# Kernel optimization log

Measured on AMD Instinct MI355X. Metric: run time of the kernel, lower is better.

The kernel has to match this reference:

```python
import jax, jax.numpy as jnp
import numpy as np

B = 8            # graphs per batch
NUM_NODES = 12500  # nodes per graph
N = B * NUM_NODES  # 100000 total nodes
E = 1_600_000      # edges (avg degree 16)
F_IN = 128
HID = 128


def _glorot(key, shape):
    lim = np.sqrt(6.0 / (shape[0] + shape[1])).astype(np.float32)
    return jax.random.uniform(key, shape, jnp.float32, -lim, lim)


def setup_inputs() -> dict:
    key = jax.random.key(0)
    ks = jax.random.split(key, 8)
    x = jax.random.normal(ks[0], (N, F_IN), jnp.float32)
    edge_index = jax.random.randint(ks[1], (2, E), 0, N, jnp.int32)
    batch = jnp.repeat(jnp.arange(B, dtype=jnp.int32), NUM_NODES)
    W1 = _glorot(ks[2], (F_IN, HID)); b1 = jnp.zeros((HID,), jnp.float32)
    W2 = _glorot(ks[3], (HID, HID));  b2 = jnp.zeros((HID,), jnp.float32)
    W3 = _glorot(ks[4], (HID, 1));    b3 = jnp.zeros((1,), jnp.float32)
    return {"x": x, "edge_index": edge_index, "batch": batch,
            "W1": W1, "b1": b1, "W2": W2, "b2": b2, "W3": W3, "b3": b3}


def _gcn_norm(src, dst, n):
    """Add self-loops and compute symmetric D^-1/2 A D^-1/2 edge weights (PyG GCNConv default)."""
    loop = jnp.arange(n, dtype=src.dtype)
    s = jnp.concatenate([src, loop])
    d = jnp.concatenate([dst, loop])
    deg = jax.ops.segment_sum(jnp.ones(s.shape[0], jnp.float32), d, num_segments=n)
    dinv = jnp.where(deg > 0, jax.lax.rsqrt(deg), 0.0)
    return s, d, dinv[s] * dinv[d]


def _gcn_conv(h, W, b, s, d, norm, n):
    h = h @ W                                   # [n, out]
    msg = h[s] * norm[:, None]                  # gather + scale
    out = jax.ops.segment_sum(msg, d, num_segments=n)  # scatter-add
    return out + b


def reference(x, edge_index, batch, W1, b1, W2, b2, W3, b3):
    n = x.shape[0]
    x_last = x[:, -1]                           # == x.view(B,NUM_NODES,F)[:,:,-1] flattened
    s, d, norm = _gcn_norm(edge_index[0], edge_index[1], n)
    h = jax.nn.relu(_gcn_conv(x, W1, b1, s, d, norm, n))   # dropout is identity in eval mode
    h = jax.nn.relu(_gcn_conv(h, W2, b2, s, d, norm, n))
    h = jax.nn.relu(_gcn_conv(h, W3, b3, s, d, norm, n))   # [n, 1]
    x_res = h.reshape(B, NUM_NODES)
    return x_res + x_last.reshape(B, NUM_NODES)
```

## Files before the change

kernel.cpp:

```cpp
#include <hip/hip_runtime.h>
#include <hip/hip_bf16.h>

typedef __attribute__((ext_vector_type(8))) short short8;
typedef __attribute__((ext_vector_type(8))) __bf16 bf16x8;
typedef __attribute__((ext_vector_type(4))) float f32x4;

static __device__ __forceinline__ float bflo(unsigned u){ return __uint_as_float(u << 16); }
static __device__ __forceinline__ float bfhi(unsigned u){ return __uint_as_float(u & 0xffff0000u); }
static __device__ __forceinline__ unsigned short f2bf(float f){
  unsigned u = __float_as_uint(f);
  unsigned r = u + 0x7fffu + ((u >> 16) & 1u);
  return (unsigned short)(r >> 16);
}

#if __has_builtin(__builtin_amdgcn_cvt_pk_fp8_f32)
static __device__ __forceinline__ unsigned char f2e4m3(float f){
  return (unsigned char)(__builtin_amdgcn_cvt_pk_fp8_f32(f, 0.f, 0, false) & 0xff);
}
#else
static __device__ __forceinline__ unsigned char f2e4m3(float f){
  unsigned s = (__float_as_uint(f) >> 31) << 7;
  float a = fabsf(f);
  if (a >= 448.f) return (unsigned char)(s | 0x7e);
  if (a < 0.0009765625f) return (unsigned char)s;
  if (a >= 0.015625f){
    int e; float m = frexpf(a, &e);
    int q = (int)rintf(m * 16.f);
    int E = e - 1 + 7;
    if (q == 16){ q = 8; E++; }
    if (E >= 16) return (unsigned char)(s | 0x7e);
    return (unsigned char)(s | (E << 3) | (q - 8));
  } else {
    int q = (int)rintf(a * 512.f);
    if (q > 7) return (unsigned char)(s | 0x08);
    return (unsigned char)(s | q);
  }
}
#endif

#if __has_builtin(__builtin_amdgcn_cvt_pk_f32_fp8)
static __device__ __forceinline__ float4 e4m3x4_to_f32(unsigned u){
  auto lo = __builtin_amdgcn_cvt_pk_f32_fp8((int)u, false);
  auto hi = __builtin_amdgcn_cvt_pk_f32_fp8((int)u, true);
  return make_float4(lo[0], lo[1], hi[0], hi[1]);
}
#else
static __device__ __forceinline__ float e4m3_1(unsigned b){
  unsigned s = b >> 7, e = (b >> 3) & 15, m = b & 7;
  float v = e ? ldexpf((float)(8 + m) * 0.125f, (int)e - 7) : ldexpf((float)m * 0.125f, -6);
  return s ? -v : v;
}
static __device__ __forceinline__ float4 e4m3x4_to_f32(unsigned u){
  return make_float4(e4m3_1(u & 255), e4m3_1((u >> 8) & 255), e4m3_1((u >> 16) & 255), e4m3_1(u >> 24));
}
#endif

static __device__ __forceinline__ void add8(float* acc, uint2 u){
  float4 a = e4m3x4_to_f32(u.x), b = e4m3x4_to_f32(u.y);
  acc[0] += a.x; acc[1] += a.y; acc[2] += a.z; acc[3] += a.w;
  acc[4] += b.x; acc[5] += b.y; acc[6] += b.z; acc[7] += b.w;
}

#define NBMAX  1024
#define PART_C 4096
#define STCAP  4096
#define BCAP   6144


__global__ __launch_bounds__(1024) void k_part(const int* __restrict__ src, const int* __restrict__ dst,
    int* __restrict__ bpos, unsigned* __restrict__ ebuf, int E, int NB)
{
  __shared__ int hist[NBMAX + 1];
  __shared__ int hist2[NBMAX];
  __shared__ int gbase[NBMAX];
  __shared__ int sc[1024];
  __shared__ unsigned staged[PART_C];
  __shared__ unsigned short sbkt[PART_C];

  const int t = threadIdx.x;
  const int base = blockIdx.x * PART_C;

  for (int i = t; i < NBMAX; i += 1024){ hist[i] = 0; hist2[i] = 0; }
  __syncthreads();

  unsigned up[4];
  int bb[4];
  #pragma unroll
  for (int j = 0; j < 4; j++){
    int e = base + j * 1024 + t;
    if (e < E){
      int s = src[e], d = dst[e];
      bb[j] = d >> 7;
      up[j] = ((unsigned)s << 7) | (unsigned)(d & 127);
      atomicAdd(&hist[bb[j]], 1);
    } else bb[j] = -1;
  }
  __syncthreads();

  int v = (t < NB) ? hist[t] : 0;
  sc[t] = v; __syncthreads();
  for (int off = 1; off < 1024; off <<= 1){
    int u = (t >= off) ? sc[t - off] : 0;
    __syncthreads();
    sc[t] += u;
    __syncthreads();
  }
  int incl = sc[t];
  if (t < NB) hist[t] = incl - v;
  if (t == NB - 1) hist[NB] = incl;
  if (t < NB && v > 0) gbase[t] = t * BCAP + atomicAdd(&bpos[t], v);
  __syncthreads();

  #pragma unroll
  for (int j = 0; j < 4; j++){
    if (bb[j] >= 0){
      int r = atomicAdd(&hist2[bb[j]], 1);
      int p = hist[bb[j]] + r;
      staged[p] = up[j];
      sbkt[p] = (unsigned short)bb[j];
    }
  }
  __syncthreads();

  int total = hist[NB];
  for (int i = t; i < total; i += 1024){
    int b = sbkt[i];
    ebuf[gbase[b] + (i - hist[b])] = staged[i];
  }
}

__global__ __launch_bounds__(256) void k_bsort(const unsigned* __restrict__ ebuf, const int* __restrict__ cnts,
    int* __restrict__ rowptr, int* __restrict__ colv, float* __restrict__ dinv, int n, int E, int NB)
{
  __shared__ int cl[128];
  __shared__ int sc2[256];
  __shared__ unsigned stg[STCAP];

  const int t = threadIdx.x;
  const int b = blockIdx.x;
  const int r0 = b << 7;
  const int rbeg = b * BCAP;
  const int total = cnts[b];

  {
    int psum = 0;
    for (int i = t; i < b; i += 256) psum += cnts[i];
    sc2[t] = psum; __syncthreads();
    for (int off = 128; off; off >>= 1){
      if (t < off) sc2[t] += sc2[t + off];
      __syncthreads();
    }
  }
  const int wbeg = sc2[0];
  __syncthreads();

  if (b == NB - 1 && t == 0) rowptr[n] = E;

  if (t < 128) cl[t] = 0;
  __syncthreads();
  for (int i = t; i < total; i += 256) atomicAdd(&cl[ebuf[rbeg + i] & 127u], 1);
  __syncthreads();

  int v = (t < 128) ? cl[t] : 0;
  sc2[t] = v; __syncthreads();
  for (int off = 1; off < 256; off <<= 1){
    int u = (t >= off) ? sc2[t - off] : 0;
    __syncthreads();
    sc2[t] += u;
    __syncthreads();
  }
  int excl = sc2[t] - v;
  if (t < 128){
    int node = r0 + t;
    if (node < n){
      rowptr[node] = wbeg + excl;
      dinv[node]   = rsqrtf((float)(v + 1));
    }
    cl[t] = excl;
  }
  __syncthreads();

  if (total <= STCAP){
    for (int i = t; i < total; i += 256){
      unsigned u = ebuf[rbeg + i];
      int p = atomicAdd(&cl[u & 127u], 1);
      stg[p] = u >> 7;
    }
    __syncthreads();
    for (int i = t; i < total; i += 256) colv[wbeg + i] = (int)stg[i];
  } else {
    for (int i = t; i < total; i += 256){
      unsigned u = ebuf[rbeg + i];
      int p = atomicAdd(&cl[u & 127u], 1);
      colv[wbeg + p] = (int)(u >> 7);
    }
  }
}


template<bool AF32>
__global__ __launch_bounds__(512) void k_gemm_mfma(const void* __restrict__ Ain, const float* __restrict__ W,
    const float* __restrict__ dinv, unsigned char* __restrict__ G8, int n)
{
  __shared__ unsigned short At[128 * 136];
  __shared__ float dl[128];

  const int t = threadIdx.x;
  const int rowBase = blockIdx.x * 128;
  const int w  = t >> 6;
  const int l  = t & 63;
  const int ln = l & 15;
  const int lg = l >> 4;

  if (t < 128){
    int gr = rowBase + t;
    dl[t] = (gr < n) ? dinv[gr] : 0.f;
  }

  #pragma unroll
  for (int i = 0; i < 4; i++){
    int flat = i * 4096 + t * 8;
    int r = flat >> 7, c = flat & 127;
    int gr = rowBase + r;
    unsigned short tmp[8];
    if constexpr (AF32){
      const float* A = (const float*)Ain;
      float4 v0 = make_float4(0.f,0.f,0.f,0.f), v1 = v0;
      if (gr < n){
        v0 = *(const float4*)(A + (size_t)gr * 128 + c);
        v1 = *(const float4*)(A + (size_t)gr * 128 + c + 4);
      }
      tmp[0]=f2bf(v0.x); tmp[1]=f2bf(v0.y); tmp[2]=f2bf(v0.z); tmp[3]=f2bf(v0.w);
      tmp[4]=f2bf(v1.x); tmp[5]=f2bf(v1.y); tmp[6]=f2bf(v1.z); tmp[7]=f2bf(v1.w);
    } else {
      const unsigned short* A = (const unsigned short*)Ain;
      short8 v = {};
      if (gr < n) v = *(const short8*)(A + (size_t)gr * 128 + c);
      *(short8*)tmp = v;
    }
    int g = (c >> 3) ^ (r & 7);
    *(short8*)((char*)At + r * 256 + g * 16) = *(const short8*)tmp;
  }

  bf16x8 bfr[4];
  #pragma unroll
  for (int kk = 0; kk < 4; kk++){
    short8 tmp;
    #pragma unroll
    for (int j = 0; j < 8; j++){
      float wv = W[(kk * 32 + lg * 8 + j) * 128 + (w * 16 + ln)];
      tmp[j] = (short)f2bf(wv);
    }
    bfr[kk] = __builtin_bit_cast(bf16x8, tmp);
  }

  f32x4 acc[8];
  #pragma unroll
  for (int m = 0; m < 8; m++) acc[m] = (f32x4){0.f,0.f,0.f,0.f};

  __syncthreads();

  #pragma unroll
  for (int m = 0; m < 8; m++){
    int row = m * 16 + ln;
    #pragma unroll
    for (int kk = 0; kk < 4; kk++){
      int g = (kk * 4 + lg) ^ (row & 7);
      short8 av = *(const short8*)((const char*)At + row * 256 + g * 16);
      acc[m] = __builtin_amdgcn_mfma_f32_16x16x32_bf16(
          __builtin_bit_cast(bf16x8, av), bfr[kk], acc[m], 0, 0, 0);
    }
  }

  __syncthreads();
  unsigned char* At8 = (unsigned char*)At;

  #pragma unroll
  for (int m = 0; m < 8; m++){
    #pragma unroll
    for (int r = 0; r < 4; r++){
      int row = m * 16 + lg * 4 + r;
      At8[row * 136 + w * 16 + ln] = f2e4m3(dl[row] * acc[m][r]);
    }
  }
  __syncthreads();

  {
    int r = t >> 2, c = (t & 3) * 32;
    int gr = rowBase + r;
    if (gr < n){
      uint4 a = *(const uint4*)(At8 + r * 136 + c);
      uint4 b = *(const uint4*)(At8 + r * 136 + c + 16);
      *(uint4*)(G8 + (size_t)gr * 128 + c)      = a;
      *(uint4*)(G8 + (size_t)gr * 128 + c + 16) = b;
    }
  }
}


template<bool LAST>
__global__ __launch_bounds__(256) void k_spmm(const uint2* __restrict__ G8, const int* __restrict__ rowptr,
    const int* __restrict__ colv, const float* __restrict__ dinv, const float* __restrict__ bias,
    const float* __restrict__ W3, unsigned* __restrict__ H, float* __restrict__ tvec, int n)
{
  int tid = blockIdx.x * 256 + threadIdx.x;
  int row = tid >> 4;
  int gl  = tid & 15;
  if (row >= n) return;

  float acc[8] = {0,0,0,0,0,0,0,0};
  add8(acc, G8[(size_t)row * 16 + gl]);
  int e = rowptr[row], e1 = rowptr[row + 1];

  for (; e + 8 <= e1; e += 8){
    int s0 = colv[e    ], s1 = colv[e + 1], s2 = colv[e + 2], s3 = colv[e + 3];
    int s4 = colv[e + 4], s5 = colv[e + 5], s6 = colv[e + 6], s7 = colv[e + 7];
    uint2 v0 = G8[(size_t)s0 * 16 + gl];
    uint2 v1 = G8[(size_t)s1 * 16 + gl];
    uint2 v2 = G8[(size_t)s2 * 16 + gl];
    uint2 v3 = G8[(size_t)s3 * 16 + gl];
    uint2 v4 = G8[(size_t)s4 * 16 + gl];
    uint2 v5 = G8[(size_t)s5 * 16 + gl];
    uint2 v6 = G8[(size_t)s6 * 16 + gl];
    uint2 v7 = G8[(size_t)s7 * 16 + gl];
    add8(acc, v0); add8(acc, v1); add8(acc, v2); add8(acc, v3);
    add8(acc, v4); add8(acc, v5); add8(acc, v6); add8(acc, v7);
  }
  for (; e + 4 <= e1; e += 4){
    int s0 = colv[e], s1 = colv[e + 1], s2 = colv[e + 2], s3 = colv[e + 3];
    uint2 v0 = G8[(size_t)s0 * 16 + gl];
    uint2 v1 = G8[(size_t)s1 * 16 + gl];
    uint2 v2 = G8[(size_t)s2 * 16 + gl];
    uint2 v3 = G8[(size_t)s3 * 16 + gl];
    add8(acc, v0); add8(acc, v1); add8(acc, v2); add8(acc, v3);
  }
  for (; e < e1; ++e) add8(acc, G8[(size_t)colv[e] * 16 + gl]);

  float dv = dinv[row];
  float r[8];
  {
    float4 b0 = *(const float4*)(bias + gl * 8);
    float4 b1 = *(const float4*)(bias + gl * 8 + 4);
    r[0] = fmaxf(fmaf(dv, acc[0], b0.x), 0.f);
    r[1] = fmaxf(fmaf(dv, acc[1], b0.y), 0.f);
    r[2] = fmaxf(fmaf(dv, acc[2], b0.z), 0.f);
    r[3] = fmaxf(fmaf(dv, acc[3], b0.w), 0.f);
    r[4] = fmaxf(fmaf(dv, acc[4], b1.x), 0.f);
    r[5] = fmaxf(fmaf(dv, acc[5], b1.y), 0.f);
    r[6] = fmaxf(fmaf(dv, acc[6], b1.z), 0.f);
    r[7] = fmaxf(fmaf(dv, acc[7], b1.w), 0.f);
  }

  if constexpr (!LAST){
    uint4 o;
    o.x = (unsigned)f2bf(r[0]) | ((unsigned)f2bf(r[1]) << 16);
    o.y = (unsigned)f2bf(r[2]) | ((unsigned)f2bf(r[3]) << 16);
    o.z = (unsigned)f2bf(r[4]) | ((unsigned)f2bf(r[5]) << 16);
    o.w = (unsigned)f2bf(r[6]) | ((unsigned)f2bf(r[7]) << 16);
    *(uint4*)(H + (size_t)row * 64 + gl * 4) = o;
  } else {
    float4 w0 = *(const float4*)(W3 + gl * 8);
    float4 w1 = *(const float4*)(W3 + gl * 8 + 4);
    float s = r[0]*w0.x + r[1]*w0.y + r[2]*w0.z + r[3]*w0.w
            + r[4]*w1.x + r[5]*w1.y + r[6]*w1.z + r[7]*w1.w;
    s += __shfl_xor(s, 1); s += __shfl_xor(s, 2);
    s += __shfl_xor(s, 4); s += __shfl_xor(s, 8);
    if (gl == 0) tvec[row] = dv * s;
  }
}


__global__ __launch_bounds__(256) void k_final3(const float* __restrict__ tvec, const int* __restrict__ rowptr,
    const int* __restrict__ colv, const float* __restrict__ dinv, const float* __restrict__ b3,
    const float* __restrict__ x, float* __restrict__ out, int n)
{
  int tid = blockIdx.x * 256 + threadIdx.x;
  int row = tid >> 4;
  int gl  = tid & 15;
  if (row >= n) return;
  float s = 0.f;
  int e0 = rowptr[row], e1 = rowptr[row + 1];
  for (int e = e0 + gl; e < e1; e += 16) s += tvec[colv[e]];
  s += __shfl_xor(s, 1); s += __shfl_xor(s, 2);
  s += __shfl_xor(s, 4); s += __shfl_xor(s, 8);
  if (gl == 0){
    s += tvec[row];
    float v = fmaxf(fmaf(dinv[row], s, b3[0]), 0.f);
    out[row] = v + x[(size_t)row * 128 + 127];
  }
}


extern "C" void kernel_launch(void* const* d_in, const int* in_sizes, int n_in,
                              void* d_out, int out_size, void* d_ws, size_t ws_size,
                              hipStream_t stream)
{
  const float* x  = (const float*)d_in[0];
  const int*   ei = (const int*)d_in[1];
  const float* W1 = (const float*)d_in[3];
  const float* b1 = (const float*)d_in[4];
  const float* W2 = (const float*)d_in[5];
  const float* b2 = (const float*)d_in[6];
  const float* W3 = (const float*)d_in[7];
  const float* b3 = (const float*)d_in[8];
  float* out = (float*)d_out;

  const int N = in_sizes[0] / 128;
  const int E = in_sizes[1] / 2;
  const int* src = ei;
  const int* dst = ei + E;
  const int NB = (N + 127) >> 7;

  char* wsb = (char*)d_ws;
  size_t off = 0;
  auto carve = [&](size_t bytes) -> void* {
    void* p = wsb + off;
    off += bytes;
    off = (off + 255) & ~(size_t)255;
    return p;
  };
  float*    dinv   = (float*)carve((size_t)N * 4);
  int*      rowptr = (int*)carve((size_t)(N + 1) * 4);
  int*      colv   = (int*)carve((size_t)E * 4);
  int*      bpos   = (int*)carve((size_t)NB * 4);
  float*    tvec   = (float*)carve((size_t)N * 4);
  unsigned char* G8 = (unsigned char*)carve((size_t)N * 128);
  unsigned* H      = (unsigned*)carve((size_t)N * 256);
  unsigned* ebuf   = (unsigned*)H;

  hipMemsetAsync(bpos, 0, (size_t)NB * 4, stream);
  k_part  <<<(E + PART_C - 1) / PART_C, 1024, 0, stream>>>(src, dst, bpos, ebuf, E, NB);
  k_bsort <<<NB, 256, 0, stream>>>(ebuf, bpos, rowptr, colv, dinv, N, E, NB);

  k_gemm_mfma<true ><<<(N + 127) / 128, 512, 0, stream>>>(x, W1, dinv, G8, N);
  k_spmm<false><<<((size_t)N * 16 + 255) / 256, 256, 0, stream>>>((const uint2*)G8, rowptr, colv, dinv, b1, nullptr, H, nullptr, N);
  k_gemm_mfma<false><<<(N + 127) / 128, 512, 0, stream>>>(H, W2, dinv, G8, N);
  k_spmm<true ><<<((size_t)N * 16 + 255) / 256, 256, 0, stream>>>((const uint2*)G8, rowptr, colv, dinv, b2, W3, nullptr, tvec, N);
  k_final3<<<((size_t)N * 16 + 255) / 256, 256, 0, stream>>>(tvec, rowptr, colv, dinv, b3, x, out, N);
}
```

Before: 150.1 us.

## Store layer-1 activations as fp8 and use wave-shuffle scans in partitioning

The intermediate hidden activation H is now packed to fp8 e4m3 instead of bf16, which halves the bytes written by the first SpMM and read by the second GEMM. The GEMM decodes the fp8 back to bf16 before the MFMA. The edge staging buffer now aliases G8 instead of H. Separately, the block-wide LDS prefix scans and reductions in the partition and bucket-sort kernels are replaced with wave shuffle scans, which removes many __syncthreads. Storing activations in fp8 adds quantization error.

```diff
diff --git a/kernel.cpp b/kernel.cpp
--- a/kernel.cpp
+++ b/kernel.cpp
@@ -5,8 +5,6 @@
 typedef __attribute__((ext_vector_type(8))) __bf16 bf16x8;
 typedef __attribute__((ext_vector_type(4))) float f32x4;
 
-static __device__ __forceinline__ float bflo(unsigned u){ return __uint_as_float(u << 16); }
-static __device__ __forceinline__ float bfhi(unsigned u){ return __uint_as_float(u & 0xffff0000u); }
 static __device__ __forceinline__ unsigned short f2bf(float f){
   unsigned u = __float_as_uint(f);
   unsigned r = u + 0x7fffu + ((u >> 16) & 1u);
@@ -16,6 +14,11 @@
 #if __has_builtin(__builtin_amdgcn_cvt_pk_fp8_f32)
 static __device__ __forceinline__ unsigned char f2e4m3(float f){
   return (unsigned char)(__builtin_amdgcn_cvt_pk_fp8_f32(f, 0.f, 0, false) & 0xff);
+}
+static __device__ __forceinline__ unsigned pk4_fp8(float a, float b, float c, float d){
+  int v = __builtin_amdgcn_cvt_pk_fp8_f32(a, b, 0, false);
+  v = __builtin_amdgcn_cvt_pk_fp8_f32(c, d, v, true);
+  return (unsigned)v;
 }
 #else
 static __device__ __forceinline__ unsigned char f2e4m3(float f){
@@ -36,6 +39,10 @@
     return (unsigned char)(s | q);
   }
 }
+static __device__ __forceinline__ unsigned pk4_fp8(float a, float b, float c, float d){
+  return (unsigned)f2e4m3(a) | ((unsigned)f2e4m3(b) << 8)
+       | ((unsigned)f2e4m3(c) << 16) | ((unsigned)f2e4m3(d) << 24);
+}
 #endif
 
 #if __has_builtin(__builtin_amdgcn_cvt_pk_f32_fp8)
@@ -73,11 +80,13 @@
   __shared__ int hist[NBMAX + 1];
   __shared__ int hist2[NBMAX];
   __shared__ int gbase[NBMAX];
-  __shared__ int sc[1024];
+  __shared__ int wsum[16];
   __shared__ unsigned staged[PART_C];
   __shared__ unsigned short sbkt[PART_C];
 
   const int t = threadIdx.x;
+  const int lane = t & 63;
+  const int wv = t >> 6;
   const int base = blockIdx.x * PART_C;
 
   for (int i = t; i < NBMAX; i += 1024){ hist[i] = 0; hist2[i] = 0; }
@@ -98,14 +107,26 @@
   __syncthreads();
 
   int v = (t < NB) ? hist[t] : 0;
-  sc[t] = v; __syncthreads();
-  for (int off = 1; off < 1024; off <<= 1){
-    int u = (t >= off) ? sc[t - off] : 0;
-    __syncthreads();
-    sc[t] += u;
-    __syncthreads();
-  }
-  int incl = sc[t];
+  int incl = v;
+  #pragma unroll
+  for (int off = 1; off < 64; off <<= 1){
+    int u = __shfl_up(incl, off);
+    if (lane >= off) incl += u;
+  }
+  if (lane == 63) wsum[wv] = incl;
+  __syncthreads();
+  if (wv == 0){
+    int s = (lane < 16) ? wsum[lane] : 0;
+    int is = s;
+    #pragma unroll
+    for (int off = 1; off < 16; off <<= 1){
+      int u = __shfl_up(is, off);
+      if (lane >= off) is += u;
+    }
+    if (lane < 16) wsum[lane] = is - s;
+  }
+  __syncthreads();
+  incl += wsum[wv];
   if (t < NB) hist[t] = incl - v;
   if (t == NB - 1) hist[NB] = incl;
   if (t < NB && v > 0) gbase[t] = t * BCAP + atomicAdd(&bpos[t], v);
@@ -133,26 +154,24 @@
     int* __restrict__ rowptr, int* __restrict__ colv, float* __restrict__ dinv, int n, int E, int NB)
 {
   __shared__ int cl[128];
-  __shared__ int sc2[256];
+  __shared__ int wred[4];
   __shared__ unsigned stg[STCAP];
 
   const int t = threadIdx.x;
+  const int lane = t & 63;
+  const int wv = t >> 6;
   const int b = blockIdx.x;
   const int r0 = b << 7;
   const int rbeg = b * BCAP;
   const int total = cnts[b];
 
-  {
-    int psum = 0;
-    for (int i = t; i < b; i += 256) psum += cnts[i];
-    sc2[t] = psum; __syncthreads();
-    for (int off = 128; off; off >>= 1){
-      if (t < off) sc2[t] += sc2[t + off];
-      __syncthreads();
-    }
-  }
-  const int wbeg = sc2[0];
-  __syncthreads();
+  int psum = 0;
+  for (int i = t; i < b; i += 256) psum += cnts[i];
+  #pragma unroll
+  for (int off = 32; off; off >>= 1) psum += __shfl_xor(psum, off);
+  if (lane == 0) wred[wv] = psum;
+  __syncthreads();
+  const int wbeg = wred[0] + wred[1] + wred[2] + wred[3];
 
   if (b == NB - 1 && t == 0) rowptr[n] = E;
 
@@ -162,14 +181,16 @@
   __syncthreads();
 
   int v = (t < 128) ? cl[t] : 0;
-  sc2[t] = v; __syncthreads();
-  for (int off = 1; off < 256; off <<= 1){
-    int u = (t >= off) ? sc2[t - off] : 0;
-    __syncthreads();
-    sc2[t] += u;
-    __syncthreads();
-  }
-  int excl = sc2[t] - v;
+  int incl = v;
+  #pragma unroll
+  for (int off = 1; off < 64; off <<= 1){
+    int u = __shfl_up(incl, off);
+    if (lane >= off) incl += u;
+  }
+  if (lane == 63) wred[wv] = incl;
+  __syncthreads();
+  incl += (wv == 1) ? wred[0] : 0;
+  int excl = incl - v;
   if (t < 128){
     int node = r0 + t;
     if (node < n){
@@ -233,10 +254,16 @@
       tmp[0]=f2bf(v0.x); tmp[1]=f2bf(v0.y); tmp[2]=f2bf(v0.z); tmp[3]=f2bf(v0.w);
       tmp[4]=f2bf(v1.x); tmp[5]=f2bf(v1.y); tmp[6]=f2bf(v1.z); tmp[7]=f2bf(v1.w);
     } else {
-      const unsigned short* A = (const unsigned short*)Ain;
-      short8 v = {};
-      if (gr < n) v = *(const short8*)(A + (size_t)gr * 128 + c);
-      *(short8*)tmp = v;
+      const unsigned char* A = (const unsigned char*)Ain;
+      if (gr < n){
+        uint2 v8 = *(const uint2*)(A + (size_t)gr * 128 + c);
+        float4 lo = e4m3x4_to_f32(v8.x), hi = e4m3x4_to_f32(v8.y);
+        tmp[0]=f2bf(lo.x); tmp[1]=f2bf(lo.y); tmp[2]=f2bf(lo.z); tmp[3]=f2bf(lo.w);
+        tmp[4]=f2bf(hi.x); tmp[5]=f2bf(hi.y); tmp[6]=f2bf(hi.z); tmp[7]=f2bf(hi.w);
+      } else {
+        #pragma unroll
+        for (int j = 0; j < 8; j++) tmp[j] = 0;
+      }
     }
     int g = (c >> 3) ^ (r & 7);
     *(short8*)((char*)At + r * 256 + g * 16) = *(const short8*)tmp;
@@ -301,7 +328,7 @@
 template<bool LAST>
 __global__ __launch_bounds__(256) void k_spmm(const uint2* __restrict__ G8, const int* __restrict__ rowptr,
     const int* __restrict__ colv, const float* __restrict__ dinv, const float* __restrict__ bias,
-    const float* __restrict__ W3, unsigned* __restrict__ H, float* __restrict__ tvec, int n)
+    const float* __restrict__ W3, uint2* __restrict__ H, float* __restrict__ tvec, int n)
 {
   int tid = blockIdx.x * 256 + threadIdx.x;
   int row = tid >> 4;
@@ -352,12 +379,10 @@
   }
 
   if constexpr (!LAST){
-    uint4 o;
-    o.x = (unsigned)f2bf(r[0]) | ((unsigned)f2bf(r[1]) << 16);
-    o.y = (unsigned)f2bf(r[2]) | ((unsigned)f2bf(r[3]) << 16);
-    o.z = (unsigned)f2bf(r[4]) | ((unsigned)f2bf(r[5]) << 16);
-    o.w = (unsigned)f2bf(r[6]) | ((unsigned)f2bf(r[7]) << 16);
-    *(uint4*)(H + (size_t)row * 64 + gl * 4) = o;
+    uint2 o;
+    o.x = pk4_fp8(r[0], r[1], r[2], r[3]);
+    o.y = pk4_fp8(r[4], r[5], r[6], r[7]);
+    H[(size_t)row * 16 + gl] = o;
   } else {
     float4 w0 = *(const float4*)(W3 + gl * 8);
     float4 w1 = *(const float4*)(W3 + gl * 8 + 4);
@@ -425,16 +450,16 @@
   int*      bpos   = (int*)carve((size_t)NB * 4);
   float*    tvec   = (float*)carve((size_t)N * 4);
   unsigned char* G8 = (unsigned char*)carve((size_t)N * 128);
-  unsigned* H      = (unsigned*)carve((size_t)N * 256);
-  unsigned* ebuf   = (unsigned*)H;
+  unsigned char* H8 = (unsigned char*)carve((size_t)N * 128);
+  unsigned* ebuf   = (unsigned*)G8;
 
   hipMemsetAsync(bpos, 0, (size_t)NB * 4, stream);
   k_part  <<<(E + PART_C - 1) / PART_C, 1024, 0, stream>>>(src, dst, bpos, ebuf, E, NB);
   k_bsort <<<NB, 256, 0, stream>>>(ebuf, bpos, rowptr, colv, dinv, N, E, NB);
 
   k_gemm_mfma<true ><<<(N + 127) / 128, 512, 0, stream>>>(x, W1, dinv, G8, N);
-  k_spmm<false><<<((size_t)N * 16 + 255) / 256, 256, 0, stream>>>((const uint2*)G8, rowptr, colv, dinv, b1, nullptr, H, nullptr, N);
-  k_gemm_mfma<false><<<(N + 127) / 128, 512, 0, stream>>>(H, W2, dinv, G8, N);
+  k_spmm<false><<<((size_t)N * 16 + 255) / 256, 256, 0, stream>>>((const uint2*)G8, rowptr, colv, dinv, b1, nullptr, (uint2*)H8, nullptr, N);
+  k_gemm_mfma<false><<<(N + 127) / 128, 512, 0, stream>>>(H8, W2, dinv, G8, N);
   k_spmm<true ><<<((size_t)N * 16 + 255) / 256, 256, 0, stream>>>((const uint2*)G8, rowptr, colv, dinv, b2, W3, nullptr, tvec, N);
   k_final3<<<((size_t)N * 16 + 255) / 256, 256, 0, stream>>>(tvec, rowptr, colv, dinv, b3, x, out, N);
 }
```

Measured after the change: 149.3 us. Within noise of the previous version (-0.5%).
